# Kernel tuning notes

Measured on AMD Instinct MI355X. Metric: run time of the kernel, lower is better.

## Reference

```python
import jax, jax.numpy as jnp
import numpy as np

N = 16384
IN_FEATS = 256
OUT_FEATS = 256


def setup_inputs() -> dict:
    key = jax.random.key(0)
    k1, k2, k3, k4 = jax.random.split(key, 4)
    # dense (row-normalized-ish) adjacency; scaled so aggregated values stay O(1)
    graph = jax.random.uniform(k1, (N, N), dtype=jnp.float32) / N
    features = jax.random.normal(k2, (N, IN_FEATS), dtype=jnp.float32)
    # nn.Linear params: W [out, in], b [out]
    W = jax.random.normal(k3, (OUT_FEATS, IN_FEATS), dtype=jnp.float32) / np.sqrt(IN_FEATS)
    b = jax.random.normal(k4, (OUT_FEATS,), dtype=jnp.float32) * 0.01
    return {"graph": graph, "features": features, "W": W, "b": b}


def reference(graph, features, W, b):
    # h = graph @ features  (GCN-style dense neighbor aggregation)
    h = jnp.matmul(graph, features)            # [N, in_feats]
    # linear: h @ W.T + b
    h = jnp.einsum('ni,oi->no', h, W) + b      # [N, out_feats]
    # activation = relu (norm = None)
    return jax.nn.relu(h)
```

## Files before the change

kernel.cpp:

```cpp
#include <hip/hip_runtime.h>
#include <hip/hip_bf16.h>

typedef float f32x4 __attribute__((ext_vector_type(4)));
typedef short short8 __attribute__((ext_vector_type(8)));
typedef __bf16 bf16x8 __attribute__((ext_vector_type(8)));

#define N_TOT 16384
#define FEATS 256
#define BM 128
#define BK 32
#define KSPLIT 4
#define NSTEPS ((N_TOT / KSPLIT) / BK)
#define ATILE (BM * 128)
#define BTILE (FEATS * 64)

static __device__ __forceinline__ ushort f2bf(float f) {
  union { __hip_bfloat16 b; ushort u; } cv;
  cv.b = __float2bfloat16(f);
  return cv.u;
}
static __device__ __forceinline__ float bf2f(ushort u) {
  union { unsigned int i; float f; } c;
  c.i = ((unsigned int)u) << 16;
  return c.f;
}
static __device__ __forceinline__ short8 cvt8s(float4 a, float4 b) {
  short8 r = { (short)f2bf(a.x), (short)f2bf(a.y), (short)f2bf(a.z), (short)f2bf(a.w),
               (short)f2bf(b.x), (short)f2bf(b.y), (short)f2bf(b.z), (short)f2bf(b.w) };
  return r;
}
template <int AUX>
static __device__ __forceinline__ void gload_lds16(const void* g, void* l) {
  __builtin_amdgcn_global_load_lds((const __attribute__((address_space(1))) unsigned int*)g,
                                   (__attribute__((address_space(3))) unsigned int*)l,
                                   16, 0, AUX);
}

__global__ __launch_bounds__(64) void k_f2t(const float* __restrict__ feat,
                                            const float* __restrict__ W,
                                            ushort* __restrict__ F2T) {
  const int lane = threadIdx.x;
  const int rsel = lane & 15, kg = lane >> 4;
  const int mb = blockIdx.x >> 1;
  const int o0 = (blockIdx.x & 1) * 128;
  const int m0 = mb * 16;

  f32x4 acc[8] = {};
#pragma unroll
  for (int ks = 0; ks < 8; ++ks) {
    const int k0 = ks * 32 + kg * 8;
    const float4 fa0 = *(const float4*)(feat + (size_t)(m0 + rsel) * FEATS + k0);
    const float4 fa1 = *(const float4*)(feat + (size_t)(m0 + rsel) * FEATS + k0 + 4);
    const short8 af = cvt8s(fa0, fa1);
#pragma unroll
    for (int of = 0; of < 8; ++of) {
      const float4 wb0 = *(const float4*)(W + (size_t)(o0 + of * 16 + rsel) * FEATS + k0);
      const float4 wb1 = *(const float4*)(W + (size_t)(o0 + of * 16 + rsel) * FEATS + k0 + 4);
      acc[of] = __builtin_amdgcn_mfma_f32_16x16x32_bf16(
          __builtin_bit_cast(bf16x8, af), __builtin_bit_cast(bf16x8, cvt8s(wb0, wb1)),
          acc[of], 0, 0, 0);
    }
  }
#pragma unroll
  for (int of = 0; of < 8; ++of) {
    ushort4 ov = { f2bf(acc[of][0]), f2bf(acc[of][1]), f2bf(acc[of][2]), f2bf(acc[of][3]) };
    *(ushort4*)(F2T + (size_t)(o0 + of * 16 + rsel) * N_TOT + m0 + kg * 4) = ov;
  }
}

__global__ __launch_bounds__(512, 4) void k_gemm1(const float* __restrict__ graph,
                                                  const ushort* __restrict__ F2T,
                                                  ushort* __restrict__ parts) {
  __shared__ char ldsA[3][ATILE];
  __shared__ char ldsB[2][BTILE];
  const int tid = threadIdx.x;
  const int lane = tid & 63, w = tid >> 6;
  const int wm = w >> 2, wn = w & 3;
  const int rsel = lane & 15, kg = lane >> 4;

  const int b = blockIdx.x;
  const int xcd = b & 7;
  const int kb = xcd >> 1;
  const int mi = (b >> 3) | ((xcd & 1) << 6);
  const size_t m0 = (size_t)mi * BM;
  const int kbase = kb * (N_TOT / KSPLIT);
  const int ph = (b * 53) & (NSTEPS - 1);

  auto stageB = [&](int bf, int t) {
    const int k0 = kbase + t * BK;
    char* dst = &ldsB[bf][0];
#pragma unroll
    for (int j = 0; j < 2; ++j) {
      const int r0 = w * 32 + j * 16;
      const int row = r0 + (lane >> 2);
      const int c = (lane & 3) ^ (row & 3);
      gload_lds16<0>(F2T + (size_t)row * N_TOT + k0 + c * 8, dst + r0 * 64);
    }
  };
  auto stageA = [&](int bf, int t) {
    const int k0 = kbase + t * BK;
    char* dst = &ldsA[bf][0];
#pragma unroll
    for (int j = 0; j < 2; ++j) {
      const int r0 = w * 16 + j * 8;
      const int row = r0 + (lane >> 3);
      const int c = (lane & 7) ^ (row & 7);
      gload_lds16<2>(graph + (m0 + row) * (size_t)N_TOT + k0 + c * 4, dst + r0 * 128);
    }
  };

  f32x4 acc[4][4] = {};

  auto compute = [&](int bfA, int bfB) {
    const char* Ab = &ldsA[bfA][0];
    const char* Bb = &ldsB[bfB][0];
    short8 bfr[4];
#pragma unroll
    for (int nf = 0; nf < 4; ++nf) {
      const int row = wn * 64 + nf * 16 + rsel;
      const int c = kg ^ (row & 3);
      bfr[nf] = *(const short8*)(Bb + row * 64 + c * 16);
    }
#pragma unroll
    for (int mf = 0; mf < 4; ++mf) {
      const int row = wm * 64 + mf * 16 + rsel;
      const int cb = (row & 7);
      const float4 a0 = *(const float4*)(Ab + row * 128 + ((kg * 2) ^ cb) * 16);
      const float4 a1 = *(const float4*)(Ab + row * 128 + ((kg * 2 + 1) ^ cb) * 16);
      const short8 af = cvt8s(a0, a1);
#pragma unroll
      for (int nf = 0; nf < 4; ++nf)
        acc[mf][nf] = __builtin_amdgcn_mfma_f32_16x16x32_bf16(
            __builtin_bit_cast(bf16x8, af), __builtin_bit_cast(bf16x8, bfr[nf]),
            acc[mf][nf], 0, 0, 0);
    }
  };

  auto tileof = [&](int s) { return (s + ph) & (NSTEPS - 1); };

  stageA(0, tileof(0));
  stageB(0, tileof(0));
  stageA(1, tileof(1));

  for (int s = 0; s < NSTEPS - 2; ++s) {
    asm volatile("s_waitcnt vmcnt(2)" ::: "memory");
    __builtin_amdgcn_s_barrier();
    stageB((s + 1) & 1, tileof(s + 1));
    stageA((s + 2) % 3, tileof(s + 2));
    __builtin_amdgcn_sched_barrier(0);
    compute(s % 3, s & 1);
  }
  {
    const int s = NSTEPS - 2;
    asm volatile("s_waitcnt vmcnt(2)" ::: "memory");
    __builtin_amdgcn_s_barrier();
    stageB((s + 1) & 1, tileof(s + 1));
    __builtin_amdgcn_sched_barrier(0);
    compute(s % 3, s & 1);
  }
  asm volatile("s_waitcnt vmcnt(0)" ::: "memory");
  __builtin_amdgcn_s_barrier();
  compute((NSTEPS - 1) % 3, (NSTEPS - 1) & 1);

  ushort* p = parts + (size_t)kb * N_TOT * FEATS;
#pragma unroll
  for (int mf = 0; mf < 4; ++mf)
#pragma unroll
    for (int nf = 0; nf < 4; ++nf)
#pragma unroll
      for (int j = 0; j < 4; ++j) {
        const int row = wm * 64 + mf * 16 + kg * 4 + j;
        const int col = wn * 64 + nf * 16 + rsel;
        p[(m0 + row) * FEATS + col] = f2bf(acc[mf][nf][j]);
      }
}

__global__ __launch_bounds__(256) void k_reduce(const ushort* __restrict__ parts,
                                                const float* __restrict__ bias,
                                                float* __restrict__ out) {
  const size_t base = ((size_t)blockIdx.x * 256 + threadIdx.x) * 8;
  const int o0 = (int)(base & (FEATS - 1));
  float s[8] = {0, 0, 0, 0, 0, 0, 0, 0};
#pragma unroll
  for (int p = 0; p < KSPLIT; ++p) {
    const short8 v = *(const short8*)(parts + (size_t)p * N_TOT * FEATS + base);
#pragma unroll
    for (int j = 0; j < 8; ++j) s[j] += bf2f((ushort)v[j]);
  }
  const float4 b0 = *(const float4*)(bias + o0);
  const float4 b1 = *(const float4*)(bias + o0 + 4);
  float4 r0 = { fmaxf(s[0] + b0.x, 0.f), fmaxf(s[1] + b0.y, 0.f),
                fmaxf(s[2] + b0.z, 0.f), fmaxf(s[3] + b0.w, 0.f) };
  float4 r1 = { fmaxf(s[4] + b1.x, 0.f), fmaxf(s[5] + b1.y, 0.f),
                fmaxf(s[6] + b1.z, 0.f), fmaxf(s[7] + b1.w, 0.f) };
  *(float4*)(out + base) = r0;
  *(float4*)(out + base + 4) = r1;
}

extern "C" void kernel_launch(void* const* d_in, const int* in_sizes, int n_in,
                              void* d_out, int out_size, void* d_ws, size_t ws_size,
                              hipStream_t stream) {
  const float* graph = (const float*)d_in[0];
  const float* feat  = (const float*)d_in[1];
  const float* W     = (const float*)d_in[2];
  const float* bias  = (const float*)d_in[3];
  float* out = (float*)d_out;

  char* ws = (char*)d_ws;
  ushort* F2T   = (ushort*)ws;
  ushort* parts = (ushort*)(ws + (size_t)8 * 1024 * 1024);

  k_f2t<<<dim3(2048), 64, 0, stream>>>(feat, W, F2T);
  k_gemm1<<<dim3((N_TOT / BM) * KSPLIT), 512, 0, stream>>>(graph, F2T, parts);
  k_reduce<<<dim3(N_TOT * FEATS / 8 / 256), 256, 0, stream>>>(parts, bias, out);
}
```

Measured before the change: 279.2 us.

## Replace triple/double-buffered staggered pipeline with unified double-buffered stage/compute loop

```diff
diff --git a/kernel.cpp b/kernel.cpp
--- a/kernel.cpp
+++ b/kernel.cpp
@@ -11,8 +11,9 @@
 #define BK 32
 #define KSPLIT 4
 #define NSTEPS ((N_TOT / KSPLIT) / BK)
-#define ATILE (BM * 128)
-#define BTILE (FEATS * 64)
+#define LDSA_BYTES (BM * 128)
+#define LDSB_BYTES (FEATS * 64)
+#define TILE_BYTES (LDSA_BYTES + LDSB_BYTES)
 
 static __device__ __forceinline__ ushort f2bf(float f) {
   union { __hip_bfloat16 b; ushort u; } cv;
@@ -71,12 +72,10 @@
 __global__ __launch_bounds__(512, 4) void k_gemm1(const float* __restrict__ graph,
                                                   const ushort* __restrict__ F2T,
                                                   ushort* __restrict__ parts) {
-  __shared__ char ldsA[3][ATILE];
-  __shared__ char ldsB[2][BTILE];
+  __shared__ char lds[2][TILE_BYTES];
   const int tid = threadIdx.x;
   const int lane = tid & 63, w = tid >> 6;
   const int wm = w >> 2, wn = w & 3;
-  const int rsel = lane & 15, kg = lane >> 4;
 
   const int b = blockIdx.x;
   const int xcd = b & 7;
@@ -86,34 +85,33 @@
   const int kbase = kb * (N_TOT / KSPLIT);
   const int ph = (b * 53) & (NSTEPS - 1);
 
-  auto stageB = [&](int bf, int t) {
+  auto stage = [&](int bf, int t) {
     const int k0 = kbase + t * BK;
-    char* dst = &ldsB[bf][0];
+    char* ldsA = &lds[bf][0];
+    char* ldsB = &lds[bf][LDSA_BYTES];
+#pragma unroll
+    for (int j = 0; j < 2; ++j) {
+      const int r0 = w * 16 + j * 8;
+      const int row = r0 + (lane >> 3);
+      const int c = (lane & 7) ^ (row & 7);
+      gload_lds16<2>(graph + (m0 + row) * (size_t)N_TOT + k0 + c * 4, ldsA + r0 * 128);
+    }
 #pragma unroll
     for (int j = 0; j < 2; ++j) {
       const int r0 = w * 32 + j * 16;
       const int row = r0 + (lane >> 2);
       const int c = (lane & 3) ^ (row & 3);
-      gload_lds16<0>(F2T + (size_t)row * N_TOT + k0 + c * 8, dst + r0 * 64);
+      gload_lds16<0>(F2T + (size_t)row * N_TOT + k0 + c * 8, ldsB + r0 * 64);
     }
   };
-  auto stageA = [&](int bf, int t) {
-    const int k0 = kbase + t * BK;
-    char* dst = &ldsA[bf][0];
-#pragma unroll
-    for (int j = 0; j < 2; ++j) {
-      const int r0 = w * 16 + j * 8;
-      const int row = r0 + (lane >> 3);
-      const int c = (lane & 7) ^ (row & 7);
-      gload_lds16<2>(graph + (m0 + row) * (size_t)N_TOT + k0 + c * 4, dst + r0 * 128);
-    }
-  };
 
   f32x4 acc[4][4] = {};
-
-  auto compute = [&](int bfA, int bfB) {
-    const char* Ab = &ldsA[bfA][0];
-    const char* Bb = &ldsB[bfB][0];
+  const int rsel = lane & 15;
+  const int kg = lane >> 4;
+
+  auto compute = [&](int bf) {
+    const char* Ab = &lds[bf][0];
+    const char* Bb = &lds[bf][LDSA_BYTES];
     short8 bfr[4];
 #pragma unroll
     for (int nf = 0; nf < 4; ++nf) {
@@ -136,31 +134,25 @@
     }
   };
 
-  auto tileof = [&](int s) { return (s + ph) & (NSTEPS - 1); };
-
-  stageA(0, tileof(0));
-  stageB(0, tileof(0));
-  stageA(1, tileof(1));
+  stage(0, ph);
+  stage(1, (ph + 1) & (NSTEPS - 1));
 
   for (int s = 0; s < NSTEPS - 2; ++s) {
-    asm volatile("s_waitcnt vmcnt(2)" ::: "memory");
+    asm volatile("s_waitcnt vmcnt(4)" ::: "memory");
     __builtin_amdgcn_s_barrier();
-    stageB((s + 1) & 1, tileof(s + 1));
-    stageA((s + 2) % 3, tileof(s + 2));
     __builtin_amdgcn_sched_barrier(0);
-    compute(s % 3, s & 1);
-  }
-  {
-    const int s = NSTEPS - 2;
-    asm volatile("s_waitcnt vmcnt(2)" ::: "memory");
+    compute(s & 1);
     __builtin_amdgcn_s_barrier();
-    stageB((s + 1) & 1, tileof(s + 1));
-    __builtin_amdgcn_sched_barrier(0);
-    compute(s % 3, s & 1);
-  }
+    stage(s & 1, (s + 2 + ph) & (NSTEPS - 1));
+  }
+  asm volatile("s_waitcnt vmcnt(4)" ::: "memory");
+  __builtin_amdgcn_s_barrier();
+  __builtin_amdgcn_sched_barrier(0);
+  compute((NSTEPS - 2) & 1);
   asm volatile("s_waitcnt vmcnt(0)" ::: "memory");
   __builtin_amdgcn_s_barrier();
-  compute((NSTEPS - 1) % 3, (NSTEPS - 1) & 1);
+  __builtin_amdgcn_sched_barrier(0);
+  compute((NSTEPS - 1) & 1);
 
   ushort* p = parts + (size_t)kb * N_TOT * FEATS;
 #pragma unroll
@@ -169,8 +161,8 @@
     for (int nf = 0; nf < 4; ++nf)
 #pragma unroll
       for (int j = 0; j < 4; ++j) {
-        const int row = wm * 64 + mf * 16 + kg * 4 + j;
-        const int col = wn * 64 + nf * 16 + rsel;
+        const int row = wm * 64 + mf * 16 + ((lane >> 4) << 2) + j;
+        const int col = wn * 64 + nf * 16 + (lane & 15);
         p[(m0 + row) * FEATS + col] = f2bf(acc[mf][nf][j]);
       }
 }
```

After: 281.1 us. About the same (+0.7%).
